# Kernel tuning notes

Hardware: AMD Instinct MI355X
Metric: run time of the kernel (lower is better)

## Reference

```python
import jax, jax.numpy as jnp
import numpy as np
import math

B, L, DIM = 128, 192, 512
NTOKEN = 100
MAX_BONDS = 6
MAX_LEN = 192


def _sinusoidal_pe(max_len, dim):
    pos = np.arange(max_len, dtype=np.float32)[:, None]
    div = np.exp(np.arange(0, dim, 2, dtype=np.float32) * (-math.log(10000.0) / dim))
    pe = np.zeros((max_len, dim), dtype=np.float32)
    pe[:, 0::2] = np.sin(pos * div)
    pe[:, 1::2] = np.cos(pos * div)
    return jnp.asarray(pe[:, None, :])  # [max_len, 1, dim]


def setup_inputs() -> dict:
    key = jax.random.key(0)
    ks = jax.random.split(key, 16)
    s = 0.02
    inp = {
        "element": jax.random.randint(ks[0], (B, L), 0, NTOKEN),
        "bond": jax.random.randint(ks[1], (B, L, MAX_BONDS), 0, L),
        "aroma": jax.random.randint(ks[2], (B, L), 0, 2),
        "charge": jax.random.randint(ks[3], (B, L), 0, 6),
        "segment": jax.random.randint(ks[4], (B, L), 0, 30),
        # parameters
        "pe": _sinusoidal_pe(MAX_LEN, DIM),
        "E_elem": jax.random.normal(ks[5], (NTOKEN, DIM), jnp.float32) * s,
        "E_charge": jax.random.normal(ks[6], (13, DIM), jnp.float32) * s,
        "E_aroma": jax.random.normal(ks[7], (2, DIM), jnp.float32) * s,
        "E_seg": jax.random.normal(ks[8], (30, DIM), jnp.float32) * s,
        "W1": jax.random.normal(ks[9], (DIM, 4 * DIM), jnp.float32) * s,
        "b1": jnp.zeros((4 * DIM,), jnp.float32),
        "W2": jax.random.normal(ks[10], (4 * DIM, DIM), jnp.float32) * s,
        "b2": jnp.zeros((DIM,), jnp.float32),
        "W3": jax.random.normal(ks[11], (DIM, 4 * DIM), jnp.float32) * s,
        "b3": jnp.zeros((4 * DIM,), jnp.float32),
        "W4": jax.random.normal(ks[12], (4 * DIM, DIM), jnp.float32) * s,
        "b4": jnp.zeros((DIM,), jnp.float32),
        "W5": jax.random.normal(ks[13], (DIM, DIM), jnp.float32) * s,
        "b5": jnp.zeros((DIM,), jnp.float32),
    }
    return inp


def _mlp(x, W1, b1, W2, b2, W3, b3, W4, b4, W5, b5):
    x = x + jnp.maximum(x @ W1 + b1, 0.0) @ W2 + b2
    x = x + jnp.maximum(x @ W3 + b3, 0.0) @ W4 + b4
    return x @ W5 + b5


def reference(element, bond, aroma, charge, segment, pe,
              E_elem, E_charge, E_aroma, E_seg,
              W1, b1, W2, b2, W3, b3, W4, b4, W5, b5):
    b, l = element.shape
    # embeddings: all [l, b, dim]
    emb = E_elem[element.T]
    emb = emb + pe[:l]                      # [l,1,dim] broadcast (eval: dropout off)
    emb = emb + E_aroma[aroma.T]
    emb = emb + E_charge[charge.T + 6]
    emb = emb + E_seg[segment.T]
    message = _mlp(emb, W1, b1, W2, b2, W3, b3, W4, b4, W5, b5)  # [l,b,dim]
    # bond aggregation: agg[k] = sum_m message[bond[b,k,m]] excluding self-bonds
    # (equivalent to the dense one-hot einsum with the diagonal masked out)
    msg_bld = jnp.transpose(message, (1, 0, 2))          # [b,l,dim]
    g = msg_bld[jnp.arange(b)[:, None, None], bond]      # [b,l,MAX_BONDS,dim]
    mask = (bond != jnp.arange(l)[None, :, None]).astype(message.dtype)
    agg = jnp.einsum('bkmd,bkm->bkd', g, mask)           # [b,l,dim]
    return emb + jnp.transpose(agg, (1, 0, 2))           # [l,b,dim]
```

## Files before the change

kernel.cpp:

```cpp
#include <hip/hip_runtime.h>
#include <cstdint>
#include <cstddef>

typedef unsigned short u16;
typedef unsigned int u32;

typedef unsigned short u16x8 __attribute__((ext_vector_type(8)));
typedef __bf16 bf16x8 __attribute__((ext_vector_type(8)));
typedef float f32x4 __attribute__((ext_vector_type(4)));
typedef float f32x8 __attribute__((ext_vector_type(8)));

#define NB   128
#define NL   192
#define NTOK (NB * NL)
#define DIM  512
#define HID  2048

static __device__ __forceinline__ float bf2f(u16 h) {
    union { u32 u; float f; } v; v.u = ((u32)h) << 16; return v.f;
}
static __device__ __forceinline__ u16 f2bf(float f) {
    union { float f; u32 u; } v; v.f = f;
    u32 u = v.u + 0x7FFF + ((v.u >> 16) & 1);
    return (u16)(u >> 16);
}

__global__ void transpose_all(const float* __restrict__ W1, u16* __restrict__ W1T,
                              const float* __restrict__ W2, u16* __restrict__ W2T,
                              const float* __restrict__ W3, u16* __restrict__ W3T,
                              const float* __restrict__ W4, u16* __restrict__ W4T,
                              const float* __restrict__ W5, u16* __restrict__ W5T) {
    int bid = blockIdx.x;
    const float* in; u16* out; int K, N, t;
    if (bid < 1024)      { in = W1; out = W1T; K = DIM; N = HID; t = bid; }
    else if (bid < 2048) { in = W2; out = W2T; K = HID; N = DIM; t = bid - 1024; }
    else if (bid < 3072) { in = W3; out = W3T; K = DIM; N = HID; t = bid - 2048; }
    else if (bid < 4096) { in = W4; out = W4T; K = HID; N = DIM; t = bid - 3072; }
    else                 { in = W5; out = W5T; K = DIM; N = DIM; t = bid - 4096; }
    const int nx = N >> 5;
    const int n0 = (t % nx) * 32, k0 = (t / nx) * 32;
    __shared__ float tile[32][33];
    int tx = threadIdx.x & 31, ty = threadIdx.x >> 5;
#pragma unroll
    for (int i = 0; i < 4; i++)
        tile[ty + i * 8][tx] = in[(size_t)(k0 + ty + i * 8) * N + n0 + tx];
    __syncthreads();
#pragma unroll
    for (int i = 0; i < 4; i++)
        out[(size_t)(n0 + ty + i * 8) * K + k0 + tx] = f2bf(tile[tx][ty + i * 8]);
}

static __device__ __forceinline__ void add8f(float* acc, const float* p) {
    f32x8 v = *(const f32x8*)p;
#pragma unroll
    for (int i = 0; i < 8; i++) acc[i] += v[i];
}

__global__ void embed_kernel(const int* __restrict__ element, const int* __restrict__ aroma,
                             const int* __restrict__ charge, const int* __restrict__ segment,
                             const float* __restrict__ pe, const float* __restrict__ E_elem,
                             const float* __restrict__ E_charge, const float* __restrict__ E_aroma,
                             const float* __restrict__ E_seg,
                             u16* __restrict__ emb16) {
    int t = blockIdx.x * 4 + (threadIdx.x >> 6);
    int lane = threadIdx.x & 63;
    int l = t >> 7, b = t & 127;
    int d = lane * 8;
    int idx = b * NL + l;
    int e = element[idx];
    int a = aroma[idx];
    int c = charge[idx] + 6;
    int s = segment[idx];
    float acc[8] = {0, 0, 0, 0, 0, 0, 0, 0};
    add8f(acc, E_elem  + (size_t)e * DIM + d);
    add8f(acc, pe      + (size_t)l * DIM + d);
    add8f(acc, E_aroma + (size_t)a * DIM + d);
    add8f(acc, E_charge+ (size_t)c * DIM + d);
    add8f(acc, E_seg   + (size_t)s * DIM + d);
    u16x8 o16;
#pragma unroll
    for (int i = 0; i < 8; i++) o16[i] = f2bf(acc[i]);
    *(u16x8*)(emb16 + (size_t)t * DIM + d) = o16;
}

__global__ __launch_bounds__(512, 2) void gemm_bt(
    const u16* __restrict__ A, const u16* __restrict__ BT,
    const float* __restrict__ bias, const u16* __restrict__ resid16,
    u16* __restrict__ C, int M, int N, int K, int do_relu) {
    __shared__ __align__(16) u16 smem[81920];

    const int tid  = threadIdx.x;
    const int wave = tid >> 6;
    const int lane = tid & 63;

    const int nwg = gridDim.x;
    const int bid = blockIdx.x;
    const int wg  = ((nwg & 7) == 0) ? ((bid & 7) * (nwg >> 3) + (bid >> 3)) : bid;
    const int nt  = N >> 8;
    const int m0  = (wg / nt) * 256;
    const int n0  = (wg % nt) * 256;

    const int wmh = wave >> 2;
    const int wnq = wave & 3;
    const int fr  = lane & 15;
    const int fq  = lane >> 4;
    const int ck0 = ((fq ^ (fr & 7)) * 8);
    const int ck1 = (((4 | fq) ^ (fr & 7)) * 8);

    const int sRow = tid >> 3;
    const int sChk = ((tid & 7) ^ (sRow & 7)) * 8;
    const int ldst = sRow * 64 + (tid & 7) * 8;

    const u16* Asrc = A  + (size_t)(m0 + sRow) * K + sChk;
    const u16* Bsrc = BT + (size_t)(n0 + sRow) * K + sChk;

    f32x4 acc[8][4] = {};

#define GLL(gp, lp) __builtin_amdgcn_global_load_lds(                            \
        (const __attribute__((address_space(1))) void*)(gp),                     \
        (__attribute__((address_space(3))) void*)(lp), 16, 0, 0)
#define STAGE_A(buf, kt) do {                                                    \
    GLL(Asrc + (size_t)(kt) * 64,                 &smem[(buf)*16384 +         ldst]); \
    GLL(Asrc + (size_t)(kt) * 64 + (size_t) 64*K, &smem[(buf)*16384 +  4096 + ldst]); \
    GLL(Asrc + (size_t)(kt) * 64 + (size_t)128*K, &smem[(buf)*16384 +  8192 + ldst]); \
    GLL(Asrc + (size_t)(kt) * 64 + (size_t)192*K, &smem[(buf)*16384 + 12288 + ldst]); \
} while (0)
#define STAGE_B(buf, kt) do {                                                    \
    GLL(Bsrc + (size_t)(kt) * 64,                 &smem[49152 + (buf)*16384 +         ldst]); \
    GLL(Bsrc + (size_t)(kt) * 64 + (size_t) 64*K, &smem[49152 + (buf)*16384 +  4096 + ldst]); \
    GLL(Bsrc + (size_t)(kt) * 64 + (size_t)128*K, &smem[49152 + (buf)*16384 +  8192 + ldst]); \
    GLL(Bsrc + (size_t)(kt) * 64 + (size_t)192*K, &smem[49152 + (buf)*16384 + 12288 + ldst]); \
} while (0)

    const int nk = K >> 6;
    STAGE_A(0, 0); STAGE_B(0, 0); STAGE_A(1, 1);

    int bt3 = 0;
    for (int t = 0; t < nk; ++t) {
        if (t < nk - 1)
            asm volatile("s_waitcnt vmcnt(4)\n\ts_barrier" ::: "memory");
        else
            asm volatile("s_waitcnt vmcnt(0)\n\ts_barrier" ::: "memory");
        if (t + 1 < nk) STAGE_B((t + 1) & 1, t + 1);
        if (t + 2 < nk) {
            int a3 = bt3 + 2; if (a3 >= 3) a3 -= 3;
            STAGE_A(a3, t + 2);
        }

        const u16* Ab = &smem[bt3 * 16384];
        const u16* Bb = &smem[49152 + (t & 1) * 16384];
#pragma unroll
        for (int s = 0; s < 2; ++s) {
            const int ck = s ? ck1 : ck0;
            bf16x8 af[8], bg[4];
#pragma unroll
            for (int i = 0; i < 8; ++i)
                af[i] = *(const bf16x8*)(&Ab[(wmh * 128 + i * 16 + fr) * 64 + ck]);
#pragma unroll
            for (int j = 0; j < 4; ++j)
                bg[j] = *(const bf16x8*)(&Bb[(wnq * 64 + j * 16 + fr) * 64 + ck]);

            __builtin_amdgcn_s_setprio(1);
#pragma unroll
            for (int i = 0; i < 8; ++i)
#pragma unroll
                for (int j = 0; j < 4; ++j)
                    acc[i][j] = __builtin_amdgcn_mfma_f32_16x16x32_bf16(
                        af[i], bg[j], acc[i][j], 0, 0, 0);
            __builtin_amdgcn_s_setprio(0);
        }
        bt3 = (bt3 == 2) ? 0 : bt3 + 1;
    }
#undef STAGE_A
#undef STAGE_B
#undef GLL

    __syncthreads();
#define CSTR 264
#pragma unroll
    for (int j = 0; j < 4; j++) {
        int n = n0 + wnq * 64 + j * 16 + fr;
        float bv = bias[n];
#pragma unroll
        for (int i = 0; i < 8; i++) {
#pragma unroll
            for (int r = 0; r < 4; r++) {
                int m = m0 + wmh * 128 + i * 16 + fq * 4 + r;
                float v = acc[i][j][r] + bv;
                if (do_relu) v = fmaxf(v, 0.0f);
                if (resid16) v += bf2f(resid16[(size_t)m * N + n]);
                smem[(wmh * 128 + i * 16 + fq * 4 + r) * CSTR + wnq * 64 + j * 16 + fr] = f2bf(v);
            }
        }
    }
    __syncthreads();
    {
        const int erow = tid >> 5;
        const int ecol = (tid & 31) * 8;
#pragma unroll
        for (int rr = 0; rr < 16; ++rr) {
            int row = rr * 16 + erow;
            *(u16x8*)(C + (size_t)(m0 + row) * N + n0 + ecol) =
                *(const u16x8*)(&smem[row * CSTR + ecol]);
        }
    }
#undef CSTR
}

__global__ void agg_kernel(const u16* __restrict__ emb16, const u16* __restrict__ msg,
                           const int* __restrict__ bond, float* __restrict__ out) {
    int t = blockIdx.x * 4 + (threadIdx.x >> 6);
    int lane = threadIdx.x & 63;
    int l = t >> 7, b = t & 127;
    int d = lane * 8;
    float acc[8];
    {
        u16x8 v = *(const u16x8*)(emb16 + (size_t)t * DIM + d);
#pragma unroll
        for (int i = 0; i < 8; i++) acc[i] = bf2f(v[i]);
    }
    const int* bp = bond + ((size_t)b * NL + l) * 6;
#pragma unroll
    for (int m = 0; m < 6; m++) {
        int j = bp[m];
        if (j != l) {
            u16x8 g = *(const u16x8*)(msg + ((size_t)j * NB + b) * DIM + d);
#pragma unroll
            for (int i = 0; i < 8; i++) acc[i] += bf2f(g[i]);
        }
    }
    f32x8 o;
#pragma unroll
    for (int i = 0; i < 8; i++) o[i] = acc[i];
    *(f32x8*)(out + (size_t)t * DIM + d) = o;
}

extern "C" void kernel_launch(void* const* d_in, const int* in_sizes, int n_in,
                              void* d_out, int out_size, void* d_ws, size_t ws_size,
                              hipStream_t stream) {
    const int* element = (const int*)d_in[0];
    const int* bond    = (const int*)d_in[1];
    const int* aroma   = (const int*)d_in[2];
    const int* charge  = (const int*)d_in[3];
    const int* segment = (const int*)d_in[4];
    const float* pe      = (const float*)d_in[5];
    const float* E_elem  = (const float*)d_in[6];
    const float* E_charge= (const float*)d_in[7];
    const float* E_aroma = (const float*)d_in[8];
    const float* E_seg   = (const float*)d_in[9];
    const float* W1 = (const float*)d_in[10];
    const float* b1 = (const float*)d_in[11];
    const float* W2 = (const float*)d_in[12];
    const float* b2 = (const float*)d_in[13];
    const float* W3 = (const float*)d_in[14];
    const float* b3 = (const float*)d_in[15];
    const float* W4 = (const float*)d_in[16];
    const float* b4 = (const float*)d_in[17];
    const float* W5 = (const float*)d_in[18];
    const float* b5 = (const float*)d_in[19];

    char* ws = (char*)d_ws;
    size_t woff = 0;
    auto take = [&](size_t bytes) -> u16* {
        u16* p = (u16*)(ws + woff);
        woff += (bytes + 255) & ~(size_t)255;
        return p;
    };
    u16* W1T = take((size_t)HID * DIM * 2);
    u16* W2T = take((size_t)DIM * HID * 2);
    u16* W3T = take((size_t)HID * DIM * 2);
    u16* W4T = take((size_t)DIM * HID * 2);
    u16* W5T = take((size_t)DIM * DIM * 2);
    u16* emb16 = take((size_t)NTOK * DIM * 2);
    u16* msg   = take((size_t)NTOK * DIM * 2);

    static const int ncs[] = {1, 2, 3, 4, 6, 8, 12, 16, 24, 32, 48, 96};
    int CM = 256;
    for (int nc : ncs) {
        int cm = NTOK / nc;
        if (cm % 256 != 0) continue;
        size_t need = woff + ((size_t)cm * HID * 2 + 256)
                           + ((size_t)cm * DIM * 2 + 256) * 2;
        if (need <= ws_size) { CM = cm; break; }
    }
    u16* hC  = take((size_t)CM * HID * 2);
    u16* xaC = take((size_t)CM * DIM * 2);
    u16* xbC = take((size_t)CM * DIM * 2);

    transpose_all<<<4352, 256, 0, stream>>>(W1, W1T, W2, W2T, W3, W3T,
                                            W4, W4T, W5, W5T);

    embed_kernel<<<NTOK / 4, 256, 0, stream>>>(element, aroma, charge, segment, pe,
                                               E_elem, E_charge, E_aroma, E_seg,
                                               emb16);

    for (int c0 = 0; c0 < NTOK; c0 += CM) {
        const u16* x16 = emb16 + (size_t)c0 * DIM;
        u16* msgC = msg + (size_t)c0 * DIM;
        int mt = CM / 256;
        gemm_bt<<<dim3(mt * (HID / 256)), 512, 0, stream>>>(x16, W1T, b1, nullptr, hC,  CM, HID, DIM, 1);
        gemm_bt<<<dim3(mt * (DIM / 256)), 512, 0, stream>>>(hC,  W2T, b2, x16,    xaC, CM, DIM, HID, 0);
        gemm_bt<<<dim3(mt * (HID / 256)), 512, 0, stream>>>(xaC, W3T, b3, nullptr, hC,  CM, HID, DIM, 1);
        gemm_bt<<<dim3(mt * (DIM / 256)), 512, 0, stream>>>(hC,  W4T, b4, xaC,    xbC, CM, DIM, HID, 0);
        gemm_bt<<<dim3(mt * (DIM / 256)), 512, 0, stream>>>(xbC, W5T, b5, nullptr, msgC, CM, DIM, DIM, 0);
    }

    agg_kernel<<<NTOK / 4, 256, 0, stream>>>(emb16, msg, bond, (float*)d_out);
}
```

Measured before the change: 453.2 us.

## Add double-buffered GEMM variant for K=512 layers, keep deep pipeline for K=2048

Adds a second GEMM kernel that double-buffers 64-wide K tiles and uses a smaller shared memory footprint (256x264 u16). The original deeper-pipelined kernel is renamed and kept for the two K=2048 projections (W2, W4). The new kernel handles the K=512 projections (W1, W3, W5). The intent is to cut prologue and pipeline-fill overhead on short-K GEMMs, possibly with better occupancy from less LDS. The tradeoff is more kernel code and less latency hiding per tile.

New measurement: 455.8 us. No clear change (+0.6%).

```diff
diff --git a/kernel.cpp b/kernel.cpp
--- a/kernel.cpp
+++ b/kernel.cpp
@@ -84,6 +84,118 @@
 }
 
 __global__ __launch_bounds__(512, 2) void gemm_bt(
+    const u16* __restrict__ A, const u16* __restrict__ BT,
+    const float* __restrict__ bias, const u16* __restrict__ resid16,
+    u16* __restrict__ C, int M, int N, int K, int do_relu) {
+    __shared__ __align__(16) u16 smem[256 * 264];
+
+    const int tid  = threadIdx.x;
+    const int wave = tid >> 6;
+    const int lane = tid & 63;
+
+    const int nwg = gridDim.x;
+    const int bid = blockIdx.x;
+    const int wg  = ((nwg & 7) == 0) ? ((bid & 7) * (nwg >> 3) + (bid >> 3)) : bid;
+    const int nt  = N >> 8;
+    const int m0  = (wg / nt) * 256;
+    const int n0  = (wg % nt) * 256;
+
+    const int wmh = wave >> 2;
+    const int wnq = wave & 3;
+    const int fr  = lane & 15;
+    const int fq  = lane >> 4;
+    const int ck0 = ((fq ^ (fr & 7)) * 8);
+    const int ck1 = (((4 | fq) ^ (fr & 7)) * 8);
+
+    const int sRow = tid >> 3;
+    const int sChk = ((tid & 7) ^ (sRow & 7)) * 8;
+    const int ldst = sRow * 64 + (tid & 7) * 8;
+
+    const u16* Asrc = A  + (size_t)(m0 + sRow) * K + sChk;
+    const u16* Bsrc = BT + (size_t)(n0 + sRow) * K + sChk;
+
+    f32x4 acc[8][4] = {};
+
+#define GLL(gp, lp) __builtin_amdgcn_global_load_lds(                            \
+        (const __attribute__((address_space(1))) void*)(gp),                     \
+        (__attribute__((address_space(3))) void*)(lp), 16, 0, 0)
+#define STAGE(buf, kt) do {                                                      \
+    GLL(Asrc + (size_t)(kt) * 64,                 &smem[(buf)*16384 +        ldst]); \
+    GLL(Bsrc + (size_t)(kt) * 64,                 &smem[32768 + (buf)*16384 +        ldst]); \
+    GLL(Asrc + (size_t)(kt) * 64 + (size_t) 64*K, &smem[(buf)*16384 +  4096 + ldst]); \
+    GLL(Bsrc + (size_t)(kt) * 64 + (size_t) 64*K, &smem[32768 + (buf)*16384 +  4096 + ldst]); \
+    GLL(Asrc + (size_t)(kt) * 64 + (size_t)128*K, &smem[(buf)*16384 +  8192 + ldst]); \
+    GLL(Bsrc + (size_t)(kt) * 64 + (size_t)128*K, &smem[32768 + (buf)*16384 +  8192 + ldst]); \
+    GLL(Asrc + (size_t)(kt) * 64 + (size_t)192*K, &smem[(buf)*16384 + 12288 + ldst]); \
+    GLL(Bsrc + (size_t)(kt) * 64 + (size_t)192*K, &smem[32768 + (buf)*16384 + 12288 + ldst]); \
+} while (0)
+
+    const int nk = K >> 6;
+    STAGE(0, 0);
+
+    for (int t = 0; t < nk; ++t) {
+        asm volatile("s_waitcnt vmcnt(0)\n\ts_barrier" ::: "memory");
+        if (t + 1 < nk) STAGE((t + 1) & 1, t + 1);
+
+        const u16* Ab = &smem[(t & 1) * 16384];
+        const u16* Bb = &smem[32768 + (t & 1) * 16384];
+#pragma unroll
+        for (int s = 0; s < 2; ++s) {
+            const int ck = s ? ck1 : ck0;
+            bf16x8 af[8], bg[4];
+#pragma unroll
+            for (int i = 0; i < 8; ++i)
+                af[i] = *(const bf16x8*)(&Ab[(wmh * 128 + i * 16 + fr) * 64 + ck]);
+#pragma unroll
+            for (int j = 0; j < 4; ++j)
+                bg[j] = *(const bf16x8*)(&Bb[(wnq * 64 + j * 16 + fr) * 64 + ck]);
+
+            __builtin_amdgcn_s_setprio(1);
+#pragma unroll
+            for (int i = 0; i < 8; ++i)
+#pragma unroll
+                for (int j = 0; j < 4; ++j)
+                    acc[i][j] = __builtin_amdgcn_mfma_f32_16x16x32_bf16(
+                        af[i], bg[j], acc[i][j], 0, 0, 0);
+            __builtin_amdgcn_s_setprio(0);
+        }
+    }
+#undef STAGE
+#undef GLL
+
+    __syncthreads();
+#define CSTR 264
+#pragma unroll
+    for (int j = 0; j < 4; j++) {
+        int n = n0 + wnq * 64 + j * 16 + fr;
+        float bv = bias[n];
+#pragma unroll
+        for (int i = 0; i < 8; i++) {
+#pragma unroll
+            for (int r = 0; r < 4; r++) {
+                int m = m0 + wmh * 128 + i * 16 + fq * 4 + r;
+                float v = acc[i][j][r] + bv;
+                if (do_relu) v = fmaxf(v, 0.0f);
+                if (resid16) v += bf2f(resid16[(size_t)m * N + n]);
+                smem[(wmh * 128 + i * 16 + fq * 4 + r) * CSTR + wnq * 64 + j * 16 + fr] = f2bf(v);
+            }
+        }
+    }
+    __syncthreads();
+    {
+        const int erow = tid >> 5;
+        const int ecol = (tid & 31) * 8;
+#pragma unroll
+        for (int rr = 0; rr < 16; ++rr) {
+            int row = rr * 16 + erow;
+            *(u16x8*)(C + (size_t)(m0 + row) * N + n0 + ecol) =
+                *(const u16x8*)(&smem[row * CSTR + ecol]);
+        }
+    }
+#undef CSTR
+}
+
+__global__ __launch_bounds__(512, 2) void gemm_bt_deep(
     const u16* __restrict__ A, const u16* __restrict__ BT,
     const float* __restrict__ bias, const u16* __restrict__ resid16,
     u16* __restrict__ C, int M, int N, int K, int do_relu) {
@@ -298,11 +410,11 @@
         const u16* x16 = emb16 + (size_t)c0 * DIM;
         u16* msgC = msg + (size_t)c0 * DIM;
         int mt = CM / 256;
-        gemm_bt<<<dim3(mt * (HID / 256)), 512, 0, stream>>>(x16, W1T, b1, nullptr, hC,  CM, HID, DIM, 1);
-        gemm_bt<<<dim3(mt * (DIM / 256)), 512, 0, stream>>>(hC,  W2T, b2, x16,    xaC, CM, DIM, HID, 0);
-        gemm_bt<<<dim3(mt * (HID / 256)), 512, 0, stream>>>(xaC, W3T, b3, nullptr, hC,  CM, HID, DIM, 1);
-        gemm_bt<<<dim3(mt * (DIM / 256)), 512, 0, stream>>>(hC,  W4T, b4, xaC,    xbC, CM, DIM, HID, 0);
-        gemm_bt<<<dim3(mt * (DIM / 256)), 512, 0, stream>>>(xbC, W5T, b5, nullptr, msgC, CM, DIM, DIM, 0);
+        gemm_bt     <<<dim3(mt * (HID / 256)), 512, 0, stream>>>(x16, W1T, b1, nullptr, hC,  CM, HID, DIM, 1);
+        gemm_bt_deep<<<dim3(mt * (DIM / 256)), 512, 0, stream>>>(hC,  W2T, b2, x16,    xaC, CM, DIM, HID, 0);
+        gemm_bt     <<<dim3(mt * (HID / 256)), 512, 0, stream>>>(xaC, W3T, b3, nullptr, hC,  CM, HID, DIM, 1);
+        gemm_bt_deep<<<dim3(mt * (DIM / 256)), 512, 0, stream>>>(hC,  W4T, b4, xaC,    xbC, CM, DIM, HID, 0);
+        gemm_bt     <<<dim3(mt * (DIM / 256)), 512, 0, stream>>>(xbC, W5T, b5, nullptr, msgC, CM, DIM, DIM, 0);
     }
 
     agg_kernel<<<NTOK / 4, 256, 0, stream>>>(emb16, msg, bond, (float*)d_out);
```
